# Kernel optimization log

Measured on AMD Instinct MI355X. Metric: run time of the kernel, lower is better.

## Reference

```python
import jax, jax.numpy as jnp
import numpy as np

B, C_IN, C_OUT, H, W = 2, 16, 16, 256, 256
DF, HID, NB = 4, 64, 3
EPS = 1e-5


def setup_inputs() -> dict:
    key = jax.random.key(0)
    ks = iter(jax.random.split(key, 64))
    def rn(shape, s=0.05):
        return jax.random.normal(next(ks), shape, jnp.float32) * s
    C5 = HID * 5
    inp = dict(
        x=jax.random.uniform(next(ks), (B, C_IN, H, W), jnp.float32),
        conv0_w=rn((HID, C_IN, 3, 3)), conv0_b=jnp.zeros((HID,)),
        prelu0=jnp.float32(0.25),
        blk_c1_w=rn((NB, C5, HID, 1, 1)), blk_c1_b=jnp.zeros((NB, C5)),
        blk_bn1_g=jnp.ones((NB, C5)), blk_bn1_b=jnp.zeros((NB, C5)),
        blk_p1=jnp.full((NB,), 0.25),
        blk_dw_w=rn((NB, C5, 1, 3, 3)), blk_dw_b=jnp.zeros((NB, C5)),
        blk_bn2_g=jnp.ones((NB, C5)), blk_bn2_b=jnp.zeros((NB, C5)),
        blk_p2=jnp.full((NB,), 0.25),
        blk_c3_w=rn((NB, HID, C5, 1, 1)), blk_c3_b=jnp.zeros((NB, HID)),
        blk_bn3_g=jnp.ones((NB, HID)), blk_bn3_b=jnp.zeros((NB, HID)),
        blk_p3=jnp.full((NB,), 0.25),
        head_w=rn((2 * C_OUT * C_IN, HID, 1, 1)), head_b=jnp.zeros((2 * C_OUT * C_IN,)),
        out_bn_g=jnp.ones((C_OUT,)), out_bn_b=jnp.zeros((C_OUT,)),
    )
    return {k: jnp.asarray(v, jnp.float32) for k, v in inp.items()}


def _conv(x, w, b, pad, groups=1):
    y = jax.lax.conv_general_dilated(x, w, (1, 1), [(pad, pad), (pad, pad)],
                                     feature_group_count=groups,
                                     dimension_numbers=('NCHW', 'OIHW', 'NCHW'))
    return y + b[None, :, None, None]


def _bn(x, g, b):  # training-mode BatchNorm2d (biased var), as torch default
    m = x.mean((0, 2, 3), keepdims=True)
    v = ((x - m) ** 2).mean((0, 2, 3), keepdims=True)
    return g[None, :, None, None] * (x - m) * jax.lax.rsqrt(v + EPS) + b[None, :, None, None]


def _prelu(x, a):
    return jnp.where(x >= 0, x, a * x)


def _corners(p, n):
    p0 = jnp.clip(jnp.floor(p), 0, n - 1)
    i0 = p0.astype(jnp.int32)
    i1 = jnp.minimum(i0 + 1, n - 1)
    return i0, i1, p - p0


def reference(x, conv0_w, conv0_b, prelu0,
              blk_c1_w, blk_c1_b, blk_bn1_g, blk_bn1_b, blk_p1,
              blk_dw_w, blk_dw_b, blk_bn2_g, blk_bn2_b, blk_p2,
              blk_c3_w, blk_c3_b, blk_bn3_g, blk_bn3_b, blk_p3,
              head_w, head_b, out_bn_g, out_bn_b):
    Bn, Ci, Hh, Ww = x.shape
    Hd, Wd = Hh // DF, Ww // DF
    # AvgPool2d(DF)
    xd = x.reshape(Bn, Ci, Hd, DF, Wd, DF).mean((3, 5))
    # predictor
    h = _prelu(_conv(xd, conv0_w, conv0_b, 1), prelu0)
    C5 = HID * 5
    for i in range(NB):
        t = _prelu(_bn(_conv(h, blk_c1_w[i], blk_c1_b[i], 0), blk_bn1_g[i], blk_bn1_b[i]), blk_p1[i])
        t = _prelu(_bn(_conv(t, blk_dw_w[i], blk_dw_b[i], 1, groups=C5), blk_bn2_g[i], blk_bn2_b[i]), blk_p2[i])
        t = _prelu(_bn(_conv(t, blk_c3_w[i], blk_c3_b[i], 0), blk_bn3_g[i], blk_bn3_b[i]), blk_p3[i])
        h = h + t
    grid = _conv(h, head_w, head_b, 0)                      # (B, 2*Co*Ci, Hd, Wd)
    grid = grid.reshape(Bn, C_OUT, Ci, 2, Hd, Wd).transpose(0, 1, 3, 4, 5, 2)  # (B,Co,2,Hd,Wd,Ci)
    gvol = grid.transpose(0, 3, 4, 5, 1, 2)                 # (B,Hd,Wd,Ci,Co,2)
    # trilinear slice (align_corners=True, border padding), matching torch
    # grid_sample axis mapping: z->Hd, y->Wd, x->Ci
    guide = jnp.clip(x, 0.0, 1.0)
    pz = jnp.clip(guide * (Hd - 1), 0.0, Hd - 1)            # (B,Ci,H,W)
    py = jnp.arange(Hh, dtype=x.dtype) / (Hh - 1) * (Wd - 1)  # (H,)
    px = jnp.arange(Ww, dtype=x.dtype) / (Ww - 1) * (Ci - 1)  # (W,)
    z0, z1, fz = _corners(pz, Hd)
    y0, y1, fy = _corners(py, Wd)
    x0, x1, fx = _corners(px, Ci)
    bI = jnp.arange(Bn)[:, None, None, None]
    fyb = fy[None, None, :, None]
    fxb = fx[None, None, None, :]
    coef = 0.0
    for zi, wz in ((z0, 1 - fz), (z1, fz)):
        for yi, wy in ((y0, 1 - fyb), (y1, fyb)):
            for xi, wx in ((x0, 1 - fxb), (x1, fxb)):
                w8 = wz * wy * wx                            # (B,Ci,H,W)
                vals = gvol[bI, zi, yi[None, None, :, None], xi[None, None, None, :]]  # (B,Ci,H,W,Co,2)
                coef = coef + vals * w8[..., None, None]
    weight = coef[..., 0]                                   # (B,Ci,H,W,Co)
    bias = coef[..., 1]
    out = jnp.einsum('bihwo,bihw->bohw', weight, x) + bias.mean(1).transpose(0, 3, 1, 2)
    out = _bn(out, out_bn_g, out_bn_b)
    return out * jax.nn.sigmoid(out)                        # SiLU
```

## Files before the change

### kernel.cpp

```cpp
#include <hip/hip_runtime.h>
#include <math.h>

namespace {

constexpr int Bn=2, CIc=16, COc=16, Hc=256, Wc=256, HIDc=64, C5c=320;
constexpr int SPc = 4096;
constexpr float EPSc = 1e-5f;

__global__ void k_down(const float* __restrict__ x, float* __restrict__ xd){
  int idx = blockIdx.x*blockDim.x + threadIdx.x;
  if (idx >= Bn*CIc*SPc) return;
  int q = idx & 63, p = (idx>>6)&63, c = idx>>12;
  const float* xp = x + ((size_t)c*Hc + p*4)*Wc + q*4;
  float s = 0.f;
  #pragma unroll
  for(int dy=0; dy<4; dy++)
    #pragma unroll
    for(int dx=0; dx<4; dx++) s += xp[dy*Wc+dx];
  xd[idx] = s * (1.f/16.f);
}

__global__ void k_conv0(const float* __restrict__ xd, const float* __restrict__ w,
                        const float* __restrict__ bias, const float* __restrict__ a0,
                        float* __restrict__ h){
  int idx = blockIdx.x*blockDim.x + threadIdx.x;
  if (idx >= Bn*HIDc*SPc) return;
  int q = idx&63, p=(idx>>6)&63, co=(idx>>12)&63, b=idx/(HIDc*SPc);
  float acc = bias[co];
  for(int ci=0; ci<CIc; ci++){
    const float* xp = xd + (size_t)(b*CIc+ci)*SPc;
    const float* wp = w + (co*CIc+ci)*9;
    #pragma unroll
    for(int u=0; u<3; u++){
      int pp = p+u-1; if((unsigned)pp >= 64u) continue;
      #pragma unroll
      for(int v=0; v<3; v++){
        int qq = q+v-1; if((unsigned)qq >= 64u) continue;
        acc = fmaf(xp[pp*64+qq], wp[u*3+v], acc);
      }
    }
  }
  float a = a0[0];
  h[idx] = acc >= 0.f ? acc : a*acc;
}

__global__ void k_c1(const float* __restrict__ h, const float* __restrict__ w,
                     const float* __restrict__ bias, float* __restrict__ t1,
                     float* __restrict__ pacc){
  __shared__ float lh[64*64];
  int og = blockIdx.x, sj = blockIdx.y, b = blockIdx.z;
  int tid = threadIdx.x;
  for(int it=0; it<4; ++it){
    int f4 = tid + it*256;
    int c = f4>>4, s4 = f4&15;
    float4 v = *(const float4*)(h + (size_t)(b*64+c)*SPc + sj*64 + s4*4);
    *(float4*)(&lh[c*64 + s4*4]) = v;
  }
  __syncthreads();
  int sq = tid & 15, oj = tid >> 4;
  int ob = og*80 + oj*5;
  float acc[4][5];
  #pragma unroll
  for(int k=0;k<4;k++)
    #pragma unroll
    for(int j=0;j<5;j++) acc[k][j] = 0.f;
  const float* lhs = lh + sq*4;
  for(int c=0;c<64;c++){
    float h0 = lhs[c*64+0];
    float h1 = lhs[c*64+1];
    float h2 = lhs[c*64+2];
    float h3 = lhs[c*64+3];
    #pragma unroll
    for(int j=0;j<5;j++){
      float wv = w[(ob+j)*64 + c];
      acc[0][j] = fmaf(h0, wv, acc[0][j]);
      acc[1][j] = fmaf(h1, wv, acc[1][j]);
      acc[2][j] = fmaf(h2, wv, acc[2][j]);
      acc[3][j] = fmaf(h3, wv, acc[3][j]);
    }
  }
  #pragma unroll
  for(int j=0;j<5;j++){
    int o = ob + j;
    float bv = bias[o];
    float4 v4 = make_float4(acc[0][j]+bv, acc[1][j]+bv, acc[2][j]+bv, acc[3][j]+bv);
    *(float4*)(t1 + (size_t)(b*320+o)*SPc + sj*64 + sq*4) = v4;
    float sm  = (v4.x+v4.y)+(v4.z+v4.w);
    float sq2 = (v4.x*v4.x + v4.y*v4.y) + (v4.z*v4.z + v4.w*v4.w);
    sm += __shfl_xor(sm,1); sq2 += __shfl_xor(sq2,1);
    sm += __shfl_xor(sm,2); sq2 += __shfl_xor(sq2,2);
    sm += __shfl_xor(sm,4); sq2 += __shfl_xor(sq2,4);
    sm += __shfl_xor(sm,8); sq2 += __shfl_xor(sq2,8);
    if(sq==0){
      pacc[o*128 + b*64 + sj]         = sm;
      pacc[40960 + o*128 + b*64 + sj] = sq2;
    }
  }
}

__global__ void k_fin(const float* __restrict__ pacc, int P, float invN,
                      const float* __restrict__ g, const float* __restrict__ bb,
                      float* __restrict__ A, float* __restrict__ B){
  __shared__ double sh[256], sh2[256];
  int c = blockIdx.x, C = gridDim.x, tid = threadIdx.x;
  double s=0.0, s2=0.0;
  for(int p=tid; p<P; p+=256){
    s  += (double)pacc[c*P+p];
    s2 += (double)pacc[C*P + c*P + p];
  }
  sh[tid]=s; sh2[tid]=s2; __syncthreads();
  for(int off=128; off>0; off>>=1){
    if(tid<off){ sh[tid]+=sh[tid+off]; sh2[tid]+=sh2[tid+off]; }
    __syncthreads();
  }
  if(tid==0){
    float m = (float)(sh[0]*(double)invN);
    float v = (float)(sh2[0]*(double)invN) - m*m;
    float r = rsqrtf(v + EPSc);
    float gc = g[c];
    A[c] = gc*r;
    B[c] = bb[c] - m*gc*r;
  }
}

__global__ void k_dw_s(const float* __restrict__ t1, const float* __restrict__ w,
                       const float* __restrict__ bias, const float* __restrict__ g1,
                       const float* __restrict__ bb1, const float* __restrict__ ap,
                       const float* __restrict__ pin, float* __restrict__ t2,
                       float* __restrict__ pout){
  int tid = threadIdx.x;
  int idx = blockIdx.x*256 + tid;
  int q = idx&63, p=(idx>>6)&63, c=(idx>>12)%C5c, b=idx/(C5c*SPc);
  __shared__ float sAB[2];
  __shared__ float ws4[4];
  {
    float v = (tid<128) ? pin[c*128 + tid] : pin[40960 + c*128 + (tid-128)];
    #pragma unroll
    for(int d=1; d<64; d<<=1) v += __shfl_xor(v, d);
    int wv = tid>>6, ln = tid&63;
    if(ln==0) ws4[wv] = v;
    __syncthreads();
    if(tid==0){
      float S = ws4[0]+ws4[1], Q = ws4[2]+ws4[3];
      float m = S*(1.f/8192.f);
      float var = Q*(1.f/8192.f) - m*m;
      float r = rsqrtf(var + EPSc);
      float gc = g1[c];
      sAB[0] = gc*r; sAB[1] = bb1[c] - m*gc*r;
    }
    __syncthreads();
  }
  float a1 = sAB[0], b1 = sAB[1], al = ap[0];
  const float* ip = t1 + (size_t)(b*C5c+c)*SPc;
  const float* wp = w + c*9;
  float acc = bias[c];
  #pragma unroll
  for(int u=0; u<3; u++){
    int pp = p+u-1; if((unsigned)pp >= 64u) continue;
    #pragma unroll
    for(int v=0; v<3; v++){
      int qq = q+v-1; if((unsigned)qq >= 64u) continue;
      float y = fmaf(ip[pp*64+qq], a1, b1);
      y = y >= 0.f ? y : al*y;
      acc = fmaf(y, wp[u*3+v], acc);
    }
  }
  t2[idx] = acc;
  float sm = acc, sq = acc*acc;
  #pragma unroll
  for(int d=1; d<64; d<<=1){ sm += __shfl_xor(sm,d); sq += __shfl_xor(sq,d); }
  __shared__ float sred[8];
  int wv = tid>>6, ln = tid&63;
  if(ln==0){ sred[wv]=sm; sred[4+wv]=sq; }
  __syncthreads();
  if(tid==0){
    float S = ((sred[0]+sred[1])+(sred[2]+sred[3]));
    float Q = ((sred[4]+sred[5])+(sred[6]+sred[7]));
    int j = blockIdx.x & 15;
    pout[c*32 + b*16 + j]         = S;
    pout[10240 + c*32 + b*16 + j] = Q;
  }
}

__global__ void k_c3f(const float* __restrict__ t2, const float* __restrict__ w,
                      const float* __restrict__ bias, const float* __restrict__ g2,
                      const float* __restrict__ bb2, const float* __restrict__ ap,
                      const float* __restrict__ pin, float* __restrict__ ts,
                      float* __restrict__ pout){
  __shared__ float sA[320], sB[320];
  __shared__ float li[320*32];
  int sjf = blockIdx.x, b = blockIdx.y;
  int tid = threadIdx.x;
  for(int c = tid; c < 320; c += 256){
    const float4* ps = (const float4*)(pin + c*32);
    const float4* pq = (const float4*)(pin + 10240 + c*32);
    float S=0.f, Q=0.f;
    #pragma unroll
    for(int j=0;j<8;j++){ float4 a = ps[j]; S += ((a.x+a.y)+(a.z+a.w)); }
    #pragma unroll
    for(int j=0;j<8;j++){ float4 a = pq[j]; Q += ((a.x+a.y)+(a.z+a.w)); }
    float m = S*(1.f/8192.f);
    float var = Q*(1.f/8192.f) - m*m;
    float r = rsqrtf(var + EPSc);
    float gc = g2[c];
    sA[c] = gc*r; sB[c] = bb2[c] - m*gc*r;
  }
  __syncthreads();
  float al = ap[0];
  for(int t = tid; t < 2560; t += 256){
    int c = t>>3, f8 = t&7;
    float4 v = *(const float4*)(t2 + (size_t)(b*C5c+c)*SPc + sjf*32 + f8*4);
    float a1 = sA[c], b1 = sB[c];
    float4 y;
    y.x = fmaf(v.x, a1, b1); y.x = y.x>=0.f ? y.x : al*y.x;
    y.y = fmaf(v.y, a1, b1); y.y = y.y>=0.f ? y.y : al*y.y;
    y.z = fmaf(v.z, a1, b1); y.z = y.z>=0.f ? y.z : al*y.z;
    y.w = fmaf(v.w, a1, b1); y.w = y.w>=0.f ? y.w : al*y.w;
    *(float4*)(&li[c*32 + f8*4]) = y;
  }
  __syncthreads();
  int sq = tid & 15, oj = tid >> 4;
  float acc[2][4];
  #pragma unroll
  for(int k=0;k<2;k++)
    #pragma unroll
    for(int j=0;j<4;j++) acc[k][j] = 0.f;
  const float* wb = w + (size_t)(oj*4)*C5c;
  const float* lis = li + sq*2;
  for(int c=0; c<320; c++){
    float h0 = lis[c*32];
    float h1 = lis[c*32+1];
    #pragma unroll
    for(int j=0;j<4;j++){
      float wv = wb[j*C5c + c];
      acc[0][j] = fmaf(h0, wv, acc[0][j]);
      acc[1][j] = fmaf(h1, wv, acc[1][j]);
    }
  }
  #pragma unroll
  for(int j=0;j<4;j++){
    int o = oj*4+j;
    float bv = bias[o];
    float v0 = acc[0][j]+bv, v1 = acc[1][j]+bv;
    *(float2*)(ts + (size_t)(b*64+o)*SPc + sjf*32 + sq*2) = make_float2(v0, v1);
    float sm = v0+v1, sq2 = v0*v0 + v1*v1;
    sm += __shfl_xor(sm,1); sq2 += __shfl_xor(sq2,1);
    sm += __shfl_xor(sm,2); sq2 += __shfl_xor(sq2,2);
    sm += __shfl_xor(sm,4); sq2 += __shfl_xor(sq2,4);
    sm += __shfl_xor(sm,8); sq2 += __shfl_xor(sq2,8);
    if(sq==0){
      pout[o*256 + b*128 + sjf]         = sm;
      pout[16384 + o*256 + b*128 + sjf] = sq2;
    }
  }
}

__global__ void k_addres(const float* __restrict__ ts, float* __restrict__ h,
                         const float* __restrict__ g3, const float* __restrict__ bb3,
                         const float* __restrict__ ap, const float* __restrict__ pin){
  int tid = threadIdx.x;
  int idx = blockIdx.x*256 + tid;
  int c = (idx>>12)&63;
  __shared__ float sAB[2];
  __shared__ float w8[8];
  {
    float S = pin[c*256 + tid];
    float Q = pin[16384 + c*256 + tid];
    #pragma unroll
    for(int d=1; d<64; d<<=1){ S += __shfl_xor(S,d); Q += __shfl_xor(Q,d); }
    int wv = tid>>6, ln = tid&63;
    if(ln==0){ w8[wv] = S; w8[4+wv] = Q; }
    __syncthreads();
    if(tid==0){
      float Sa = (w8[0]+w8[1])+(w8[2]+w8[3]);
      float Qa = (w8[4]+w8[5])+(w8[6]+w8[7]);
      float m = Sa*(1.f/8192.f);
      float var = Qa*(1.f/8192.f) - m*m;
      float r = rsqrtf(var + EPSc);
      float gc = g3[c];
      sAB[0] = gc*r; sAB[1] = bb3[c] - m*gc*r;
    }
    __syncthreads();
  }
  float y = fmaf(ts[idx], sAB[0], sAB[1]);
  float al = ap[0];
  y = y >= 0.f ? y : al*y;
  h[idx] += y;
}

__global__ void k_head_t(const float* __restrict__ h, const float* __restrict__ w,
                         const float* __restrict__ bias, float* __restrict__ gv){
  __shared__ float lh[8*65];
  __shared__ float lw[64*65];
  int bid = blockIdx.x;
  int pgg = bid & 7, q = (bid>>3) & 63, b = bid >> 9;
  int tid = threadIdx.x;
  for(int t = tid; t < 512; t += 256){
    int p = t >> 6, kc = t & 63;
    lh[p*65 + kc] = h[((size_t)(b*64+kc))*SPc + (pgg*8+p)*64 + q];
  }
  int cc = tid & 63, pp = tid >> 6;
  float* gb = gv + (size_t)b*(64*16*2048) + ((size_t)q*16)*2048;
  for(int ch = 0; ch < 8; ++ch){
    __syncthreads();
    for(int t = tid; t < 1024; t += 256){
      int rc = t >> 4, f4 = t & 15;
      int combo = ch*64 + rc;
      int ci = combo>>5, kk = (combo>>4)&1, o = combo&15;
      int c0 = (o*16+ci)*2 + kk;
      float4 v = *(const float4*)(w + (size_t)c0*64 + f4*4);
      *(float4*)(&lw[rc*65 + f4*4]) = v;
    }
    __syncthreads();
    int combo = ch*64 + cc;
    int ci = combo>>5, kk = (combo>>4)&1, o = combo&15;
    int c0 = (o*16+ci)*2 + kk;
    float a0 = 0.f, a1 = 0.f;
    const float* lh0 = &lh[(pp*2+0)*65];
    const float* lh1 = &lh[(pp*2+1)*65];
    const float* lwr = &lw[cc*65];
    #pragma unroll 8
    for(int kc=0; kc<64; kc++){
      float wv = lwr[kc];
      a0 = fmaf(lh0[kc], wv, a0);
      a1 = fmaf(lh1[kc], wv, a1);
    }
    float bv = bias[c0];
    float* dst = gb + (size_t)ci*2048 + kk*1024 + o*64 + pgg*8 + pp*2;
    *(float2*)dst = make_float2(a0 + bv, a1 + bv);
  }
}

__global__ void k_slice(const float* __restrict__ x, const float* __restrict__ gv,
                        float* __restrict__ outp, float* __restrict__ pacc){
  __shared__ float lds[8320];
  int xseg = blockIdx.x, hp = blockIdx.y, b = blockIdx.z;
  int tid = threadIdx.x;
  const float* gb = gv + (size_t)b*(64*16*2048);
  int y0 = (hp*63)/255;
  int y1 = min(y0+1, 63);
  float fy = hp*(63.f/255.f) - (float)y0;

  if(tid < 128){
    int half = tid & 1, o = (tid>>1)&15, k = (tid>>5)&1, cix = (tid>>6)&1;
    int xs = min(xseg + cix, 15);
    const float* b0p = gb + (size_t)(y0*16+xs)*2048 + k*1024 + o*64;
    const float* b1p = gb + (size_t)(y1*16+xs)*2048 + k*1024 + o*64;
    float2* d = (float2*)lds + cix*2080 + k*1040 + o*65;
    float prev = 0.f;
    if(half){
      float a = b0p[31], c = b1p[31];
      prev = fmaf(fy, c-a, a);
    }
    int j0 = half*8;
    #pragma unroll
    for(int j=0; j<8; ++j){
      int jj = j0 + j;
      float4 a = *(const float4*)(b0p + jj*4);
      float4 c = *(const float4*)(b1p + jj*4);
      float v0 = fmaf(fy, c.x-a.x, a.x);
      float v1 = fmaf(fy, c.y-a.y, a.y);
      float v2 = fmaf(fy, c.z-a.z, a.z);
      float v3 = fmaf(fy, c.w-a.w, a.w);
      if(j > 0 || half) d[4*jj-1] = make_float2(prev, v0);
      d[4*jj]   = make_float2(v0, v1);
      d[4*jj+1] = make_float2(v1, v2);
      d[4*jj+2] = make_float2(v2, v3);
      prev = v3;
    }
    if(half) d[63] = make_float2(prev, prev);
  }
  __syncthreads();

  int wv = tid>>6, lane = tid&63;
  int o = lane & 15, pl = lane >> 4;
  int lc = wv*4 + pl;
  int wq = xseg*17 + lc;
  bool act = (lc < 17) && (wq < 256);
  int wqc = min(wq, 255);

  float fx = (float)lc * (1.f/17.f);
  float cwA = 1.f - fx, cwB = fx;
  int obase = o*65;
  const float2* l2 = (const float2*)lds;

  float acc = 0.f, bacc = 0.f;
  for(int i=0; i<CIc; i++){
    float xv = x[((size_t)(b*CIc+i)*Hc + hp)*Wc + wqc];
    float g = fminf(fmaxf(xv, 0.f), 1.f);
    float pz = g*63.f;
    int z0 = (int)pz; float fz = pz - (float)z0;
    float wz0 = cwA*(1.f-fz), wz1 = cwA*fz;
    float vz0 = cwB*(1.f-fz), vz1 = cwB*fz;
    int aA = obase + z0, aB = 2080 + obase + z0;
    float2 wA = l2[aA],        wB = l2[aB];
    float2 bA = l2[aA + 1040], bB = l2[aB + 1040];
    float wsum = fmaf(wz0, wA.x, fmaf(wz1, wA.y, fmaf(vz0, wB.x, vz1*wB.y)));
    float bsum = fmaf(wz0, bA.x, fmaf(wz1, bA.y, fmaf(vz0, bB.x, vz1*bB.y)));
    acc  = fmaf(xv, wsum, acc);
    bacc += bsum;
  }
  float vout = act ? (acc + bacc*(1.f/16.f)) : 0.f;
  if(act)
    outp[((size_t)(b*COc+o)*Hc + hp)*Wc + wq] = vout;

  float sm = vout, sq = vout*vout;
  sm += __shfl_xor(sm,16); sq += __shfl_xor(sq,16);
  sm += __shfl_xor(sm,32); sq += __shfl_xor(sq,32);
  __syncthreads();
  if(lane < 16){ lds[(wv*16+o)*2] = sm; lds[(wv*16+o)*2+1] = sq; }
  __syncthreads();
  if(tid < 32){
    int oo = tid>>1, kd = tid&1;
    float S = (((lds[(0*16+oo)*2+kd] + lds[(1*16+oo)*2+kd])
             +  (lds[(2*16+oo)*2+kd] + lds[(3*16+oo)*2+kd]))
             +   lds[(4*16+oo)*2+kd]);
    int blk = (b*256 + hp)*16 + xseg;
    pacc[kd*131072 + oo*8192 + blk] = S;
  }
}

__global__ void k_final(float* __restrict__ out, const float* __restrict__ A,
                        const float* __restrict__ B){
  int idx = blockIdx.x*256 + threadIdx.x;
  int c = (idx>>16)&15;
  float y = fmaf(out[idx], A[c], B[c]);
  out[idx] = y / (1.f + expf(-y));
}

}

extern "C" void kernel_launch(void* const* d_in, const int* in_sizes, int n_in,
                              void* d_out, int out_size, void* d_ws, size_t ws_size,
                              hipStream_t stream){
  const float* x       = (const float*)d_in[0];
  const float* conv0_w = (const float*)d_in[1];
  const float* conv0_b = (const float*)d_in[2];
  const float* prelu0  = (const float*)d_in[3];
  const float* c1w  = (const float*)d_in[4];
  const float* c1b  = (const float*)d_in[5];
  const float* bn1g = (const float*)d_in[6];
  const float* bn1b = (const float*)d_in[7];
  const float* p1   = (const float*)d_in[8];
  const float* dww  = (const float*)d_in[9];
  const float* dwb  = (const float*)d_in[10];
  const float* bn2g = (const float*)d_in[11];
  const float* bn2b = (const float*)d_in[12];
  const float* p2   = (const float*)d_in[13];
  const float* c3w  = (const float*)d_in[14];
  const float* c3b  = (const float*)d_in[15];
  const float* bn3g = (const float*)d_in[16];
  const float* bn3b = (const float*)d_in[17];
  const float* p3   = (const float*)d_in[18];
  const float* hw   = (const float*)d_in[19];
  const float* hb   = (const float*)d_in[20];
  const float* obg  = (const float*)d_in[21];
  const float* obb  = (const float*)d_in[22];
  float* out = (float*)d_out;
  float* ws  = (float*)d_ws;

  float* xd    = ws;
  float* h     = xd + 131072;
  float* A     = h  + 524288;
  float* B     = A  + 320;
  float* pacc  = B  + 320;
  float* paccb = pacc + 81920;
  float* paccc = paccb + 20480;
  float* t1    = paccc + 65536;
  float* t2    = t1 + 2621440;
  float* ts    = t2 + 2621440;
  float* gv    = t1;
  float* pacc2 = ts;

  k_down <<<512,  256, 0, stream>>>(x, xd);
  k_conv0<<<2048, 256, 0, stream>>>(xd, conv0_w, conv0_b, prelu0, h);

  for(int i=0; i<3; i++){
    k_c1  <<<dim3(4,64,Bn), 256, 0, stream>>>(h, c1w + i*20480, c1b + i*320, t1, pacc);
    k_dw_s<<<10240, 256, 0, stream>>>(t1, dww + i*2880, dwb + i*320,
                                      bn1g+i*320, bn1b+i*320, p1+i, pacc, t2, paccb);
    k_c3f <<<dim3(128,Bn), 256, 0, stream>>>(t2, c3w + i*20480, c3b + i*64,
                                             bn2g+i*320, bn2b+i*320, p2+i, paccb, ts, paccc);
    k_addres<<<2048, 256, 0, stream>>>(ts, h, bn3g+i*64, bn3b+i*64, p3+i, paccc);
  }

  k_head_t<<<1024, 256, 0, stream>>>(h, hw, hb, gv);
  k_slice <<<dim3(16,256,Bn), 320, 0, stream>>>(x, gv, out, pacc2);
  k_fin   <<<16, 256, 0, stream>>>(pacc2, 8192, 1.f/131072.f, obg, obb, A, B);
  k_final <<<8192, 256, 0, stream>>>(out, A, B);
}
```

Measured before the change: 319.6 us.

## Tile depthwise conv per channel plane in LDS with 4x4 outputs per thread

The depthwise 3x3 conv kernel now assigns one block per (batch, channel) 64x64 plane. The plane is loaded once into padded shared memory with BN1+PReLU applied on load, and each thread computes a 4x4 output patch from it. Each input is normalized once instead of up to nine times, and redundant global loads go away. The partial-sum buffer for BN2 stats shrinks to one entry per (channel, batch), which simplifies the consumer reduction. The trade-off is a much smaller grid (640 blocks), less parallelism, and strided 4-wide output stores per thread that are only partially coalesced.

```diff
diff --git a/kernel.cpp b/kernel.cpp
--- a/kernel.cpp
+++ b/kernel.cpp
@@ -128,9 +128,10 @@
                        const float* __restrict__ bb1, const float* __restrict__ ap,
                        const float* __restrict__ pin, float* __restrict__ t2,
                        float* __restrict__ pout){
+  __shared__ float lt[64*65];
+  int bid = blockIdx.x;
+  int c = bid % C5c, b = bid / C5c;
   int tid = threadIdx.x;
-  int idx = blockIdx.x*256 + tid;
-  int q = idx&63, p=(idx>>6)&63, c=(idx>>12)%C5c, b=idx/(C5c*SPc);
   __shared__ float sAB[2];
   __shared__ float ws4[4];
   {
@@ -152,33 +153,58 @@
   }
   float a1 = sAB[0], b1 = sAB[1], al = ap[0];
   const float* ip = t1 + (size_t)(b*C5c+c)*SPc;
+  for(int t = tid; t < 1024; t += 256){
+    int p = t >> 4, f4 = t & 15;
+    float4 v = *(const float4*)(ip + p*64 + f4*4);
+    float4 y;
+    y.x = fmaf(v.x, a1, b1); y.x = y.x>=0.f ? y.x : al*y.x;
+    y.y = fmaf(v.y, a1, b1); y.y = y.y>=0.f ? y.y : al*y.y;
+    y.z = fmaf(v.z, a1, b1); y.z = y.z>=0.f ? y.z : al*y.z;
+    y.w = fmaf(v.w, a1, b1); y.w = y.w>=0.f ? y.w : al*y.w;
+    *(float4*)(&lt[p*65 + f4*4]) = y;
+  }
   const float* wp = w + c*9;
-  float acc = bias[c];
-  #pragma unroll
-  for(int u=0; u<3; u++){
-    int pp = p+u-1; if((unsigned)pp >= 64u) continue;
-    #pragma unroll
-    for(int v=0; v<3; v++){
-      int qq = q+v-1; if((unsigned)qq >= 64u) continue;
-      float y = fmaf(ip[pp*64+qq], a1, b1);
-      y = y >= 0.f ? y : al*y;
-      acc = fmaf(y, wp[u*3+v], acc);
-    }
-  }
-  t2[idx] = acc;
-  float sm = acc, sq = acc*acc;
-  #pragma unroll
-  for(int d=1; d<64; d<<=1){ sm += __shfl_xor(sm,d); sq += __shfl_xor(sq,d); }
+  float w00=wp[0], w01=wp[1], w02=wp[2],
+        w10=wp[3], w11=wp[4], w12=wp[5],
+        w20=wp[6], w21=wp[7], w22=wp[8];
+  float bv = bias[c];
+  __syncthreads();
+  int r0 = (tid >> 4) * 4, q0 = (tid & 15) * 4;
+  float sm = 0.f, sq2 = 0.f;
+  float* op = t2 + (size_t)(b*C5c+c)*SPc;
+  #pragma unroll
+  for(int dr=0; dr<4; ++dr){
+    int p = r0 + dr;
+    #pragma unroll
+    for(int dq=0; dq<4; ++dq){
+      int q = q0 + dq;
+      float acc = bv;
+      #pragma unroll
+      for(int u=0; u<3; u++){
+        int pp = p+u-1; if((unsigned)pp >= 64u) continue;
+        const float* lr = &lt[pp*65];
+        float wr0 = (u==0)?w00:(u==1)?w10:w20;
+        float wr1 = (u==0)?w01:(u==1)?w11:w21;
+        float wr2 = (u==0)?w02:(u==1)?w12:w22;
+        if(q >= 1)  acc = fmaf(lr[q-1], wr0, acc);
+        acc = fmaf(lr[q], wr1, acc);
+        if(q <= 62) acc = fmaf(lr[q+1], wr2, acc);
+      }
+      op[p*64 + q] = acc;
+      sm += acc; sq2 += acc*acc;
+    }
+  }
+  #pragma unroll
+  for(int d=1; d<64; d<<=1){ sm += __shfl_xor(sm,d); sq2 += __shfl_xor(sq2,d); }
   __shared__ float sred[8];
   int wv = tid>>6, ln = tid&63;
-  if(ln==0){ sred[wv]=sm; sred[4+wv]=sq; }
+  if(ln==0){ sred[wv]=sm; sred[4+wv]=sq2; }
   __syncthreads();
   if(tid==0){
     float S = ((sred[0]+sred[1])+(sred[2]+sred[3]));
     float Q = ((sred[4]+sred[5])+(sred[6]+sred[7]));
-    int j = blockIdx.x & 15;
-    pout[c*32 + b*16 + j]         = S;
-    pout[10240 + c*32 + b*16 + j] = Q;
+    pout[c*2 + b]       = S;
+    pout[640 + c*2 + b] = Q;
   }
 }
 
@@ -192,13 +218,8 @@
   int sjf = blockIdx.x, b = blockIdx.y;
   int tid = threadIdx.x;
   for(int c = tid; c < 320; c += 256){
-    const float4* ps = (const float4*)(pin + c*32);
-    const float4* pq = (const float4*)(pin + 10240 + c*32);
-    float S=0.f, Q=0.f;
-    #pragma unroll
-    for(int j=0;j<8;j++){ float4 a = ps[j]; S += ((a.x+a.y)+(a.z+a.w)); }
-    #pragma unroll
-    for(int j=0;j<8;j++){ float4 a = pq[j]; Q += ((a.x+a.y)+(a.z+a.w)); }
+    float S = pin[c*2] + pin[c*2+1];
+    float Q = pin[640 + c*2] + pin[640 + c*2+1];
     float m = S*(1.f/8192.f);
     float var = Q*(1.f/8192.f) - m*m;
     float r = rsqrtf(var + EPSc);
@@ -477,8 +498,8 @@
 
   for(int i=0; i<3; i++){
     k_c1  <<<dim3(4,64,Bn), 256, 0, stream>>>(h, c1w + i*20480, c1b + i*320, t1, pacc);
-    k_dw_s<<<10240, 256, 0, stream>>>(t1, dww + i*2880, dwb + i*320,
-                                      bn1g+i*320, bn1b+i*320, p1+i, pacc, t2, paccb);
+    k_dw_s<<<640, 256, 0, stream>>>(t1, dww + i*2880, dwb + i*320,
+                                    bn1g+i*320, bn1b+i*320, p1+i, pacc, t2, paccb);
     k_c3f <<<dim3(128,Bn), 256, 0, stream>>>(t2, c3w + i*20480, c3b + i*64,
                                              bn2g+i*320, bn2b+i*320, p2+i, paccb, ts, paccc);
     k_addres<<<2048, 256, 0, stream>>>(ts, h, bn3g+i*64, bn3b+i*64, p3+i, paccc);
```

Measured after the change: 288.7 us. 1.11x faster.
